# Kernel optimization log

Hardware: AMD Instinct MI355X
Metric: run time of the kernel (lower is better)

## Reference

```python
import jax, jax.numpy as jnp
import numpy as np

B, D, N, H = 1024, 512, 16, 512  # batch, latent, branches, hidden


def _lrelu(v):
    return jnp.where(v >= 0, v, 0.1 * v)  # LeakyReLU(0.1)


def setup_inputs() -> dict:
    key = jax.random.key(0)
    ks = jax.random.split(key, 9)
    s = 0.02
    return {
        "x": jax.random.normal(ks[0], (B, D, N), dtype=jnp.float32),
        "Ws1": jax.random.normal(ks[1], (D, D), dtype=jnp.float32) * s,
        "bs1": jnp.zeros((D,), dtype=jnp.float32),
        "Ws2": jax.random.normal(ks[2], (D, D), dtype=jnp.float32) * s,
        "bs2": jnp.zeros((D,), dtype=jnp.float32),
        # per-branch binary classifiers: Linear(D,H)+LeakyReLU+Linear(H,1)
        "Wc1": jax.random.normal(ks[3], (N, D, H), dtype=jnp.float32) * s,
        "bc1": jnp.zeros((N, H), dtype=jnp.float32),
        "Wc2": jax.random.normal(ks[4], (N, H), dtype=jnp.float32) * s,
        "bc2": jnp.zeros((N,), dtype=jnp.float32),
    }


def reference(x, Ws1, bs1, Ws2, bs2, Wc1, bc1, Wc2, bc2):
    # x: [B, D, N] -> per-branch tokens [B, N, D]
    xb = jnp.transpose(x, (0, 2, 1))
    # shared MLP applied to every branch slice (same weights)
    h = _lrelu(xb @ Ws1 + bs1)
    shared = _lrelu(h @ Ws2 + bs2)  # [B, N, D]
    # per-branch classifier on its own branch slice -> sigmoid probs
    h1 = _lrelu(jnp.einsum('bnd,ndh->bnh', shared, Wc1) + bc1)
    logits = jnp.einsum('bnh,nh->bn', h1, Wc2) + bc2  # [B, N]
    out = jax.nn.sigmoid(logits)[:, None, :]  # [B, 1, N]
    # full pass: concat branch slices along batch (branch-major), every
    # classifier applied to the full stack -> raw logits
    full_in = jnp.transpose(shared, (1, 0, 2)).reshape(N * B, D)  # [M, D]
    h2 = _lrelu(jnp.einsum('md,ndh->mnh', full_in, Wc1) + bc1)  # [M, N, H]
    full_logits = jnp.einsum('mnh,nh->mn', h2, Wc2) + bc2  # [M, N]
    full_out = full_logits[:, None, :]  # [N*B, 1, N]
    return (out, full_out)
```

## Files before the change

kernel.cpp:

```cpp
#include <hip/hip_runtime.h>
#include <hip/hip_bf16.h>
#include <stdint.h>

#define Bq 1024
#define Dq 512
#define Nq 16
#define Hq 512
#define Mq (Bq*Nq)

typedef short v8s  __attribute__((ext_vector_type(8)));
typedef float v16f __attribute__((ext_vector_type(16)));
typedef int   v4i  __attribute__((ext_vector_type(4)));

typedef __attribute__((address_space(3))) unsigned int as3_u32;
typedef __attribute__((address_space(1))) const unsigned int as1_u32;

__device__ __forceinline__ unsigned short f2bf(float f) {
  union { float f; unsigned u; } v; v.f = f;
  return (unsigned short)((v.u + 0x7fffu + ((v.u >> 16) & 1u)) >> 16);
}

__global__ void k_transpose_x(const float* __restrict__ x, unsigned short* __restrict__ xb) {
  __shared__ float lds[Dq][Nq + 1];
  const int b = blockIdx.x;
  const float* xi = x + (size_t)b * Dq * Nq;
  const int t = threadIdx.x;
  for (int p = 0; p < (Dq*Nq)/256; ++p) {
    int i = t + p*256;
    lds[i >> 4][i & (Nq-1)] = xi[i];
  }
  __syncthreads();
  unsigned short* o = xb + (size_t)b * Nq * Dq;
  for (int p = 0; p < (Dq*Nq)/256; ++p) {
    int i = t + p*256;
    o[i] = f2bf(lds[i & (Dq-1)][i >> 9]);
  }
}

__global__ void k_transpose_w(const float* __restrict__ Ws1, const float* __restrict__ Ws2,
                              const float* __restrict__ Wc1,
                              unsigned short* __restrict__ Ws1t, unsigned short* __restrict__ Ws2t,
                              unsigned short* __restrict__ Wc1t) {
  __shared__ float tile[32][33];
  const int z = blockIdx.z;
  const float* in;
  unsigned short* out;
  if (z == 0)      { in = Ws1; out = Ws1t; }
  else if (z == 1) { in = Ws2; out = Ws2t; }
  else             { in = Wc1 + (size_t)(z-2) * 512 * 512; out = Wc1t + (size_t)(z-2) * 512 * 512; }
  const int tx = threadIdx.x, ty = threadIdx.y;
  const int c0 = blockIdx.x * 32, r0 = blockIdx.y * 32;
#pragma unroll
  for (int j = 0; j < 4; ++j)
    tile[ty + j*8][tx] = in[(size_t)(r0 + ty + j*8) * 512 + c0 + tx];
  __syncthreads();
#pragma unroll
  for (int j = 0; j < 4; ++j) {
    int c = c0 + ty + j*8;
    int r = r0 + tx;
    out[(size_t)c * 512 + r] = f2bf(tile[tx][ty + j*8]);
  }
}

template<int MODE, int BM>
__global__ __launch_bounds__(256, 2)
void k_gemm(const unsigned short* __restrict__ A,
            const unsigned short* __restrict__ Bt,
            const float* __restrict__ bias,
            void* __restrict__ out_,
            const float* __restrict__ w2,
            int permute) {
  constexpr int BN = 128, BK = 32, KD = 512;
  constexpr int NI = (BM == 256) ? 4 : 2;
  constexpr int AG = BM / 16;
  __shared__ __align__(16) unsigned short As[BM][BK];
  __shared__ __align__(16) unsigned short Bs[BN][BK];

  const int t = threadIdx.x;
  const int wave = t >> 6, lane = t & 63;
  const int wr = (BM == 256) ? wave : (wave >> 1);
  const int wc = (BM == 256) ? 0    : (wave & 1);
  const int l32 = lane & 31, kh0 = lane >> 5;
  const int bm = blockIdx.x * BM, bn = blockIdx.y * BN;
  const int z = blockIdx.z;

  const unsigned short* Bz = Bt + (size_t)z * KD * 512;
  const float* biasz = bias + (size_t)z * 512;

  const int lrow = lane >> 2;
  const int lslot = lane & 3;

  v16f acc[2][NI] = {};

  for (int kt = 0; kt < KD / BK; ++kt) {
#pragma unroll
    for (int i = wave; i < AG + 8; i += 4) {
      const int isA = (i < AG);
      const int r0 = (isA ? i : i - AG) * 16;
      const int row = r0 + lrow;
      const int cg = lslot ^ ((row >> 1) & 3);
      const unsigned short* g = isA ? &A [(size_t)(bm + row) * KD + kt*BK + cg*8]
                                    : &Bz[(size_t)(bn + row) * KD + kt*BK + cg*8];
      as3_u32* d = isA ? (as3_u32*)&As[r0][0] : (as3_u32*)&Bs[r0][0];
      __builtin_amdgcn_global_load_lds((as1_u32*)g, d, 16, 0, 0);
    }
    __syncthreads();
    v8s af[2][2], bf[NI][2];
#pragma unroll
    for (int mi = 0; mi < 2; ++mi) {
      int ra = wr*64 + mi*32 + l32;
#pragma unroll
      for (int kh = 0; kh < 2; ++kh) {
        int c = kh*2 + kh0;
        af[mi][kh] = *(const v8s*)&As[ra][(c ^ ((ra >> 1) & 3)) * 8];
      }
    }
#pragma unroll
    for (int ni = 0; ni < NI; ++ni) {
      int rb = wc*64 + ni*32 + l32;
#pragma unroll
      for (int kh = 0; kh < 2; ++kh) {
        int c = kh*2 + kh0;
        bf[ni][kh] = *(const v8s*)&Bs[rb][(c ^ ((rb >> 1) & 3)) * 8];
      }
    }
#pragma unroll
    for (int kh = 0; kh < 2; ++kh)
#pragma unroll
      for (int mi = 0; mi < 2; ++mi)
#pragma unroll
        for (int ni = 0; ni < NI; ++ni)
          acc[mi][ni] = __builtin_amdgcn_mfma_f32_32x32x16_bf16(af[mi][kh], bf[ni][kh], acc[mi][ni], 0, 0, 0);
    __syncthreads();
  }

  if (MODE == 0) {
    unsigned short* O = (unsigned short*)out_;
#pragma unroll
    for (int mi = 0; mi < 2; ++mi) {
#pragma unroll
      for (int ni = 0; ni < NI; ++ni) {
        int col = bn + wc*64 + ni*32 + l32;
        float bcol = biasz[col];
#pragma unroll
        for (int reg = 0; reg < 16; ++reg) {
          int rl = (reg & 3) + 8*(reg >> 2) + 4*kh0;
          int grow = bm + wr*64 + mi*32 + rl;
          int orow = permute ? ((grow & 15) * Bq + (grow >> 4)) : grow;
          float v = acc[mi][ni][reg] + bcol;
          v = v >= 0.f ? v : 0.1f * v;
          O[(size_t)orow * 512 + col] = f2bf(v);
        }
      }
    }
  } else {
    float* FL = (float*)out_;
    const float* w2z = w2 + (size_t)z * 512;
#pragma unroll
    for (int mi = 0; mi < 2; ++mi) {
#pragma unroll
      for (int reg = 0; reg < 16; ++reg) {
        int rl = (reg & 3) + 8*(reg >> 2) + 4*kh0;
        float s = 0.f;
#pragma unroll
        for (int ni = 0; ni < NI; ++ni) {
          int col = bn + ni*32 + l32;
          float v = acc[mi][ni][reg] + biasz[col];
          v = v >= 0.f ? v : 0.1f * v;
          s += v * w2z[col];
        }
#pragma unroll
        for (int off = 1; off < 32; off <<= 1)
          s += __shfl_xor(s, off, 64);
        if (l32 == 0) {
          int grow = bm + wave*64 + mi*32 + rl;
          atomicAdd(&FL[(size_t)grow * Nq + z], s);
        }
      }
    }
  }
}

__global__ void k_final(const float* __restrict__ fl, const float* __restrict__ bc2,
                        float* __restrict__ out) {
  int i = blockIdx.x * 256 + threadIdx.x;
  int m = i >> 4, n = i & 15;
  float v = fl[i] + bc2[n];
  out[Mq + i] = v;
  if (n == (m >> 10)) {
    int b = m & (Bq - 1);
    out[b * Nq + n] = 1.f / (1.f + __expf(-v));
  }
}

extern "C" void kernel_launch(void* const* d_in, const int* in_sizes, int n_in,
                              void* d_out, int out_size, void* d_ws, size_t ws_size,
                              hipStream_t stream) {
  (void)in_sizes; (void)n_in; (void)out_size; (void)ws_size;
  const float* x   = (const float*)d_in[0];
  const float* Ws1 = (const float*)d_in[1];
  const float* bs1 = (const float*)d_in[2];
  const float* Ws2 = (const float*)d_in[3];
  const float* bs2 = (const float*)d_in[4];
  const float* Wc1 = (const float*)d_in[5];
  const float* bc1 = (const float*)d_in[6];
  const float* Wc2 = (const float*)d_in[7];
  const float* bc2 = (const float*)d_in[8];

  char* ws = (char*)d_ws;
  unsigned short* Xb   = (unsigned short*)(ws);
  unsigned short* Hbuf = (unsigned short*)(ws + (size_t)16*1024*1024);
  unsigned short* Sm   = (unsigned short*)(ws + (size_t)32*1024*1024);
  unsigned short* Ws1t = (unsigned short*)(ws + (size_t)48*1024*1024);
  unsigned short* Ws2t = (unsigned short*)(ws + (size_t)48*1024*1024 + 512*1024);
  unsigned short* Wc1t = (unsigned short*)(ws + (size_t)49*1024*1024);
  float*          FL   = (float*)         (ws + (size_t)57*1024*1024);

  hipMemsetAsync(FL, 0, (size_t)Mq * Nq * sizeof(float), stream);

  k_transpose_x<<<Bq, 256, 0, stream>>>(x, Xb);
  k_transpose_w<<<dim3(16,16,18), dim3(32,8), 0, stream>>>(Ws1, Ws2, Wc1, Ws1t, Ws2t, Wc1t);

  k_gemm<0,128><<<dim3(128,4,1), 256, 0, stream>>>(Xb,   Ws1t, bs1, Hbuf, nullptr, 0);
  k_gemm<0,128><<<dim3(128,4,1), 256, 0, stream>>>(Hbuf, Ws2t, bs2, Sm,   nullptr, 1);
  k_gemm<1,256><<<dim3(64,4,16), 256, 0, stream>>>(Sm, Wc1t, bc1, FL, Wc2, 0);

  k_final<<<(Mq*Nq)/256, 256, 0, stream>>>(FL, bc2, (float*)d_out);
}
```

Measured before the change: 342.6 us.

## Widen GEMM K-tile to 128 and unify on a 128x128 block tile

The GEMM K-step grows from 32 to 128, so there are 4 K iterations instead of 16 and a quarter as many barriers. The LDS swizzle is widened to 8-way to suit the longer rows. The large classifier GEMM moves from 256x128 tiles with one wave per row group to 128x128 tiles on a 2x2 wave grid, which doubles its grid size. This adds LDS use (64KB per block), which may limit occupancy. The load for the next tile is issued only after the trailing barrier, so global loads still do not overlap compute within a block.

```diff
diff --git a/kernel.cpp b/kernel.cpp
--- a/kernel.cpp
+++ b/kernel.cpp
@@ -10,7 +10,6 @@
 
 typedef short v8s  __attribute__((ext_vector_type(8)));
 typedef float v16f __attribute__((ext_vector_type(16)));
-typedef int   v4i  __attribute__((ext_vector_type(4)));
 
 typedef __attribute__((address_space(3))) unsigned int as3_u32;
 typedef __attribute__((address_space(1))) const unsigned int as1_u32;
@@ -62,7 +61,7 @@
   }
 }
 
-template<int MODE, int BM>
+template<int MODE>
 __global__ __launch_bounds__(256, 2)
 void k_gemm(const unsigned short* __restrict__ A,
             const unsigned short* __restrict__ Bt,
@@ -70,16 +69,13 @@
             void* __restrict__ out_,
             const float* __restrict__ w2,
             int permute) {
-  constexpr int BN = 128, BK = 32, KD = 512;
-  constexpr int NI = (BM == 256) ? 4 : 2;
-  constexpr int AG = BM / 16;
+  constexpr int BM = 128, BN = 128, BK = 128, KD = 512, NKT = KD / BK;
   __shared__ __align__(16) unsigned short As[BM][BK];
   __shared__ __align__(16) unsigned short Bs[BN][BK];
 
   const int t = threadIdx.x;
   const int wave = t >> 6, lane = t & 63;
-  const int wr = (BM == 256) ? wave : (wave >> 1);
-  const int wc = (BM == 256) ? 0    : (wave & 1);
+  const int wrm = wave >> 1, wrn = wave & 1;
   const int l32 = lane & 31, kh0 = lane >> 5;
   const int bm = blockIdx.x * BM, bn = blockIdx.y * BN;
   const int z = blockIdx.z;
@@ -87,51 +83,52 @@
   const unsigned short* Bz = Bt + (size_t)z * KD * 512;
   const float* biasz = bias + (size_t)z * 512;
 
-  const int lrow = lane >> 2;
-  const int lslot = lane & 3;
-
-  v16f acc[2][NI] = {};
-
-  for (int kt = 0; kt < KD / BK; ++kt) {
-#pragma unroll
-    for (int i = wave; i < AG + 8; i += 4) {
-      const int isA = (i < AG);
-      const int r0 = (isA ? i : i - AG) * 16;
-      const int row = r0 + lrow;
-      const int cg = lslot ^ ((row >> 1) & 3);
-      const unsigned short* g = isA ? &A [(size_t)(bm + row) * KD + kt*BK + cg*8]
-                                    : &Bz[(size_t)(bn + row) * KD + kt*BK + cg*8];
+  const int srow = lane >> 4;
+  const int sslot = lane & 15;
+
+  auto stage = [&](int kt) {
+#pragma unroll
+    for (int j = 0; j < 16; ++j) {
+      const int g = wave * 16 + j;
+      const bool isA = (g < 32);
+      const int r0 = (isA ? g : g - 32) * 4;
+      const int row = r0 + srow;
+      const int cg = sslot ^ ((row >> 1) & 7);
+      const unsigned short* gp = isA ? &A [(size_t)(bm + row) * KD + kt*BK + cg*8]
+                                     : &Bz[(size_t)(bn + row) * KD + kt*BK + cg*8];
       as3_u32* d = isA ? (as3_u32*)&As[r0][0] : (as3_u32*)&Bs[r0][0];
-      __builtin_amdgcn_global_load_lds((as1_u32*)g, d, 16, 0, 0);
-    }
+      __builtin_amdgcn_global_load_lds((as1_u32*)gp, d, 16, 0, 0);
+    }
+  };
+
+  v16f acc[2][2] = {};
+
+  stage(0);
+
+  for (int kt = 0; kt < NKT; ++kt) {
     __syncthreads();
-    v8s af[2][2], bf[NI][2];
-#pragma unroll
-    for (int mi = 0; mi < 2; ++mi) {
-      int ra = wr*64 + mi*32 + l32;
-#pragma unroll
-      for (int kh = 0; kh < 2; ++kh) {
-        int c = kh*2 + kh0;
-        af[mi][kh] = *(const v8s*)&As[ra][(c ^ ((ra >> 1) & 3)) * 8];
-      }
-    }
-#pragma unroll
-    for (int ni = 0; ni < NI; ++ni) {
-      int rb = wc*64 + ni*32 + l32;
-#pragma unroll
-      for (int kh = 0; kh < 2; ++kh) {
-        int c = kh*2 + kh0;
-        bf[ni][kh] = *(const v8s*)&Bs[rb][(c ^ ((rb >> 1) & 3)) * 8];
-      }
-    }
-#pragma unroll
-    for (int kh = 0; kh < 2; ++kh)
+    const int ra0 = wrm*64 + l32, rb0 = wrn*64 + l32;
+#pragma unroll
+    for (int ks = 0; ks < 8; ++ks) {
+      v8s af[2], bf[2];
+#pragma unroll
+      for (int mi = 0; mi < 2; ++mi) {
+        int ra = ra0 + mi*32;
+        af[mi] = *(const v8s*)&As[ra][(((ks*2 + kh0) ^ ((ra >> 1) & 7))) * 8];
+      }
+#pragma unroll
+      for (int ni = 0; ni < 2; ++ni) {
+        int rb = rb0 + ni*32;
+        bf[ni] = *(const v8s*)&Bs[rb][(((ks*2 + kh0) ^ ((rb >> 1) & 7))) * 8];
+      }
 #pragma unroll
       for (int mi = 0; mi < 2; ++mi)
 #pragma unroll
-        for (int ni = 0; ni < NI; ++ni)
-          acc[mi][ni] = __builtin_amdgcn_mfma_f32_32x32x16_bf16(af[mi][kh], bf[ni][kh], acc[mi][ni], 0, 0, 0);
+        for (int ni = 0; ni < 2; ++ni)
+          acc[mi][ni] = __builtin_amdgcn_mfma_f32_32x32x16_bf16(af[mi], bf[ni], acc[mi][ni], 0, 0, 0);
+    }
     __syncthreads();
+    if (kt + 1 < NKT) stage(kt + 1);
   }
 
   if (MODE == 0) {
@@ -139,13 +136,13 @@
 #pragma unroll
     for (int mi = 0; mi < 2; ++mi) {
 #pragma unroll
-      for (int ni = 0; ni < NI; ++ni) {
-        int col = bn + wc*64 + ni*32 + l32;
+      for (int ni = 0; ni < 2; ++ni) {
+        int col = bn + wrn*64 + ni*32 + l32;
         float bcol = biasz[col];
 #pragma unroll
         for (int reg = 0; reg < 16; ++reg) {
           int rl = (reg & 3) + 8*(reg >> 2) + 4*kh0;
-          int grow = bm + wr*64 + mi*32 + rl;
+          int grow = bm + wrm*64 + mi*32 + rl;
           int orow = permute ? ((grow & 15) * Bq + (grow >> 4)) : grow;
           float v = acc[mi][ni][reg] + bcol;
           v = v >= 0.f ? v : 0.1f * v;
@@ -163,8 +160,8 @@
         int rl = (reg & 3) + 8*(reg >> 2) + 4*kh0;
         float s = 0.f;
 #pragma unroll
-        for (int ni = 0; ni < NI; ++ni) {
-          int col = bn + ni*32 + l32;
+        for (int ni = 0; ni < 2; ++ni) {
+          int col = bn + wrn*64 + ni*32 + l32;
           float v = acc[mi][ni][reg] + biasz[col];
           v = v >= 0.f ? v : 0.1f * v;
           s += v * w2z[col];
@@ -173,7 +170,7 @@
         for (int off = 1; off < 32; off <<= 1)
           s += __shfl_xor(s, off, 64);
         if (l32 == 0) {
-          int grow = bm + wave*64 + mi*32 + rl;
+          int grow = bm + wrm*64 + mi*32 + rl;
           atomicAdd(&FL[(size_t)grow * Nq + z], s);
         }
       }
@@ -221,9 +218,9 @@
   k_transpose_x<<<Bq, 256, 0, stream>>>(x, Xb);
   k_transpose_w<<<dim3(16,16,18), dim3(32,8), 0, stream>>>(Ws1, Ws2, Wc1, Ws1t, Ws2t, Wc1t);
 
-  k_gemm<0,128><<<dim3(128,4,1), 256, 0, stream>>>(Xb,   Ws1t, bs1, Hbuf, nullptr, 0);
-  k_gemm<0,128><<<dim3(128,4,1), 256, 0, stream>>>(Hbuf, Ws2t, bs2, Sm,   nullptr, 1);
-  k_gemm<1,256><<<dim3(64,4,16), 256, 0, stream>>>(Sm, Wc1t, bc1, FL, Wc2, 0);
+  k_gemm<0><<<dim3(128,4,1), 256, 0, stream>>>(Xb,   Ws1t, bs1, Hbuf, nullptr, 0);
+  k_gemm<0><<<dim3(128,4,1), 256, 0, stream>>>(Hbuf, Ws2t, bs2, Sm,   nullptr, 1);
+  k_gemm<1><<<dim3(128,4,16), 256, 0, stream>>>(Sm, Wc1t, bc1, FL, Wc2, 0);
 
   k_final<<<(Mq*Nq)/256, 256, 0, stream>>>(FL, bc2, (float*)d_out);
 }
```

Result: slower. 385.3 us (+12.5%).
